# Performance work log

Measured on AMD Instinct MI355X. Metric: run time of the kernel, lower is better.

The kernel has to match this reference:

```python
import jax, jax.numpy as jnp
import numpy as np

B, T, CIN = 8, 4096, 512
GROUP, ENTRY = 2, 320
COUT = 512
D = COUT // GROUP  # per-group codebook dim = 256


def setup_inputs() -> dict:
    key = jax.random.key(0)
    k_x, k_w, k_cb, k_g = jax.random.split(key, 4)
    x = jax.random.normal(k_x, (B, T, CIN), dtype=jnp.float32)
    # weight_proj: Linear(in_channel, group*entry)
    Wp = jax.random.normal(k_w, (GROUP * ENTRY, CIN), dtype=jnp.float32) * (1.0 / np.sqrt(CIN))
    bp = jnp.zeros((GROUP * ENTRY,), dtype=jnp.float32)
    # stacked codebooks: [group, entry, out_channel//group]
    codebooks = jax.random.normal(k_cb, (GROUP, ENTRY, D), dtype=jnp.float32)
    # pre-sampled gumbel noise (torch gumbel_softmax samples this internally)
    gumbel = jax.random.gumbel(k_g, (B, T, GROUP * ENTRY), dtype=jnp.float32)
    return {"x": x, "Wp": Wp, "bp": bp, "codebooks": codebooks, "gumbel": gumbel}


def reference(x, Wp, bp, codebooks, gumbel):
    # weight_proj
    logits = jnp.einsum('btc,ec->bte', x, Wp) + bp          # [B,T,group*entry]
    # gumbel_softmax(tau=1, hard=False, dim=-1): softmax over full group*entry axis
    y = jax.nn.softmax(logits + gumbel, axis=-1)            # [B,T,group*entry]
    # chunk into groups -> contiguous reshape matches torch.chunk
    yg = y.reshape(B, T, GROUP, ENTRY)                      # [B,T,G,E]
    # per-group matmul against codebook weights, then concat over groups
    out = jnp.einsum('btge,ged->btgd', yg, codebooks)       # [B,T,G,D]
    return out.reshape(B, T, GROUP * D)                     # [B,T,out_channel]
```

## Files before the change

### kernel.cpp

```cpp
#include <hip/hip_runtime.h>
#include <hip/hip_bf16.h>
#include <stdint.h>

#define BT     32768
#define CIN    512
#define NE     640
#define ENTRY  320
#define DD     256
#define MROWS  64
#define TPB    512

using bf16x8 = __attribute__((ext_vector_type(8))) short;
using f32x4  = __attribute__((ext_vector_type(4))) float;

#define Y_OFF   0
#define Y_STR   648
#define S_OFF   82944
#define A_OFF   83200
#define A_STR   80
#define B_OFF   88320
#define CB_OFF  83200
#define SMEM_BYTES 129280

__device__ __forceinline__ unsigned short f2b(float f) {
    union { float f; uint32_t u; } v; v.f = f;
    uint32_t u = v.u;
    return (unsigned short)((u + 0x7FFFu + ((u >> 16) & 1u)) >> 16);
}

__device__ __forceinline__ void gl2lds16(const void* g, void* l) {
    __builtin_amdgcn_global_load_lds((const __attribute__((address_space(1))) void*)g,
                                     (__attribute__((address_space(3))) void*)l, 16, 0, 0);
}

__global__ void prep_kernel(const float* __restrict__ Wp, const float* __restrict__ cb,
                            unsigned short* __restrict__ WpB, unsigned short* __restrict__ cbT) {
    int i = blockIdx.x * blockDim.x + threadIdx.x;
    if (i < NE * CIN) {
        WpB[i] = f2b(Wp[i]);
    } else {
        int o = i - NE * CIN;
        if (o < 2 * ENTRY * DD) {
            int g = o / (DD * ENTRY);
            int r = o - g * (DD * ENTRY);
            int d = r / ENTRY;
            int e = r - d * ENTRY;
            cbT[o] = f2b(cb[(g * ENTRY + e) * DD + d]);
        }
    }
}

__global__ __launch_bounds__(TPB, 2) void fused_kernel(
    const float* __restrict__ x, const float* __restrict__ bp,
    const float* __restrict__ gum, const unsigned short* __restrict__ WpB,
    const unsigned short* __restrict__ cbT, float* __restrict__ out) {

    extern __shared__ char smem[];
    unsigned short* yS = (unsigned short*)(smem + Y_OFF);
    float*          sS = (float*)(smem + S_OFF);
    char*           aS = smem + A_OFF;
    char*           bS = smem + B_OFF;
    char*           cS = smem + CB_OFF;

    const int tid = threadIdx.x;
    const int w  = tid >> 6;
    const int l  = tid & 63;
    const int q  = l >> 4;
    const int ln = l & 15;
    const int rowbase = blockIdx.x * MROWS;

    if (tid < MROWS) sS[tid] = 0.0f;

    f32x4 acc1[4][5];
    const f32x4 fz = {0.f, 0.f, 0.f, 0.f};
#pragma unroll
    for (int rt = 0; rt < 4; ++rt)
#pragma unroll
        for (int ct = 0; ct < 5; ++ct) acc1[rt][ct] = fz;

    const int ar  = tid >> 3;
    const int akq = tid & 7;
    const float* xrow = x + (rowbase + ar) * CIN + akq * 4;

#pragma unroll 1
    for (int ks = 0; ks < 16; ++ks) {
        const int k0 = ks * 32;
        __syncthreads();
        float4 xv = *(const float4*)(xrow + k0);
        ushort4 hv;
        hv.x = f2b(xv.x); hv.y = f2b(xv.y); hv.z = f2b(xv.z); hv.w = f2b(xv.w);
        *(ushort4*)(aS + ar * A_STR + akq * 8) = hv;
#pragma unroll
        for (int i = 0; i < 5; ++i) {
            int cbase = i * 512 + (w << 6);
            int c = cbase + l;
            int e = c >> 2;
            int q2 = (c & 3) ^ ((e >> 1) & 3);
            gl2lds16(WpB + e * CIN + k0 + q2 * 8, bS + cbase * 16);
        }
        __syncthreads();
        bf16x8 af[4];
#pragma unroll
        for (int rt = 0; rt < 4; ++rt)
            af[rt] = *(const bf16x8*)(aS + (rt * 16 + ln) * A_STR + q * 16);
        bf16x8 bfr[5];
#pragma unroll
        for (int ct = 0; ct < 5; ++ct) {
            int e = w * 80 + ct * 16 + ln;
            int ch = e * 4 + (q ^ ((e >> 1) & 3));
            bfr[ct] = *(const bf16x8*)(bS + ch * 16);
        }
#pragma unroll
        for (int rt = 0; rt < 4; ++rt)
#pragma unroll
            for (int ct = 0; ct < 5; ++ct)
                acc1[rt][ct] = __builtin_amdgcn_mfma_f32_16x16x32_bf16(af[rt], bfr[ct], acc1[rt][ct], 0, 0, 0);
    }

    float bpv[5];
#pragma unroll
    for (int ct = 0; ct < 5; ++ct) bpv[ct] = bp[w * 80 + ct * 16 + ln];

#pragma unroll
    for (int rt = 0; rt < 4; ++rt) {
#pragma unroll
        for (int r = 0; r < 4; ++r) {
            int row = rt * 16 + q * 4 + r;
            int grow = (rowbase + row) * NE;
            float p = 0.f;
#pragma unroll
            for (int ct = 0; ct < 5; ++ct) {
                int col = w * 80 + ct * 16 + ln;
                float v = acc1[rt][ct][r] + bpv[ct] + gum[grow + col];
                float e = __expf(v);
                yS[row * Y_STR + col] = f2b(e);
                p += e;
            }
            p += __shfl_xor(p, 1);
            p += __shfl_xor(p, 2);
            p += __shfl_xor(p, 4);
            p += __shfl_xor(p, 8);
            if (ln == 0) atomicAdd(&sS[row], p);
        }
    }

    f32x4 acc2[4][4];
#pragma unroll
    for (int rt = 0; rt < 4; ++rt)
#pragma unroll
        for (int ct = 0; ct < 4; ++ct) acc2[rt][ct] = fz;

    const int g  = w >> 2;
    const int nb = (w & 3) * 64;

#pragma unroll 1
    for (int ks = 0; ks < 10; ++ks) {
        const int k0 = ks * 32;
        __syncthreads();
#pragma unroll
        for (int i = 0; i < 4; ++i) {
            int cbase = i * 512 + (w << 6);
            int c = cbase + l;
            int gg = c >> 10;
            int cc = c & 1023;
            int n = cc >> 2;
            int q2 = (cc & 3) ^ ((n >> 1) & 3);
            gl2lds16(cbT + (gg * DD + n) * ENTRY + k0 + q2 * 8, cS + cbase * 16);
        }
        __syncthreads();
        bf16x8 af[4];
#pragma unroll
        for (int rt = 0; rt < 4; ++rt)
            af[rt] = *(const bf16x8*)((char*)yS + (rt * 16 + ln) * (Y_STR * 2) + (g * ENTRY + k0 + q * 8) * 2);
        bf16x8 bfr[4];
#pragma unroll
        for (int ct = 0; ct < 4; ++ct) {
            int n = nb + ct * 16 + ln;
            int ch = (g << 10) + n * 4 + (q ^ ((n >> 1) & 3));
            bfr[ct] = *(const bf16x8*)(cS + ch * 16);
        }
#pragma unroll
        for (int rt = 0; rt < 4; ++rt)
#pragma unroll
            for (int ct = 0; ct < 4; ++ct)
                acc2[rt][ct] = __builtin_amdgcn_mfma_f32_16x16x32_bf16(af[rt], bfr[ct], acc2[rt][ct], 0, 0, 0);
    }

#pragma unroll
    for (int rt = 0; rt < 4; ++rt) {
#pragma unroll
        for (int r = 0; r < 4; ++r) {
            int row = rt * 16 + q * 4 + r;
            float inv = 1.0f / sS[row];
            int orow = (rowbase + row) * 512;
#pragma unroll
            for (int ct = 0; ct < 4; ++ct) {
                int col = g * DD + nb + ct * 16 + ln;
                out[orow + col] = acc2[rt][ct][r] * inv;
            }
        }
    }
}

extern "C" void kernel_launch(void* const* d_in, const int* in_sizes, int n_in,
                              void* d_out, int out_size, void* d_ws, size_t ws_size,
                              hipStream_t stream) {
    const float* x   = (const float*)d_in[0];
    const float* Wp  = (const float*)d_in[1];
    const float* bp  = (const float*)d_in[2];
    const float* cb  = (const float*)d_in[3];
    const float* gum = (const float*)d_in[4];
    float* out = (float*)d_out;

    unsigned short* WpB = (unsigned short*)d_ws;
    unsigned short* cbT = WpB + NE * CIN;

    int prep_total = NE * CIN + 2 * ENTRY * DD;
    prep_kernel<<<(prep_total + 255) / 256, 256, 0, stream>>>(Wp, cb, WpB, cbT);

    fused_kernel<<<dim3(BT / MROWS), dim3(TPB), SMEM_BYTES, stream>>>(x, bp, gum, WpB, cbT, out);
}
```

Measured before the change: 251.2 us.

## Stage full x tile in LDS once and stream weights directly into registers

The whole 64x512 x tile is converted to bf16 and staged into LDS once up front, replacing the per-k-step staging that needed two barriers per iteration. The Wp and codebook B-fragments are no longer copied into LDS; each wave loads them from global memory straight into registers, double-buffered one k-step ahead. Gumbel noise values are also prefetched a row ahead during the softmax epilogue. This removes most barriers and LDS traffic, at the cost of more LDS (150KB, which limits occupancy to one block per CU) and redundant global or L2 reads of the weights across waves.

```diff
diff --git a/kernel.cpp b/kernel.cpp
--- a/kernel.cpp
+++ b/kernel.cpp
@@ -12,25 +12,20 @@
 
 using bf16x8 = __attribute__((ext_vector_type(8))) short;
 using f32x4  = __attribute__((ext_vector_type(4))) float;
-
-#define Y_OFF   0
-#define Y_STR   648
-#define S_OFF   82944
-#define A_OFF   83200
-#define A_STR   80
-#define B_OFF   88320
-#define CB_OFF  83200
-#define SMEM_BYTES 129280
+using u16x8  = __attribute__((ext_vector_type(8))) unsigned short;
+
+#define X_OFF   0
+#define X_STRB  1040
+#define Y_OFF   66560
+#define Y_STRB  1296
+#define Y_STRE  648
+#define S_OFF   149504
+#define SMEM_BYTES 149760
 
 __device__ __forceinline__ unsigned short f2b(float f) {
     union { float f; uint32_t u; } v; v.f = f;
     uint32_t u = v.u;
     return (unsigned short)((u + 0x7FFFu + ((u >> 16) & 1u)) >> 16);
-}
-
-__device__ __forceinline__ void gl2lds16(const void* g, void* l) {
-    __builtin_amdgcn_global_load_lds((const __attribute__((address_space(1))) void*)g,
-                                     (__attribute__((address_space(3))) void*)l, 16, 0, 0);
 }
 
 __global__ void prep_kernel(const float* __restrict__ Wp, const float* __restrict__ cb,
@@ -58,9 +53,6 @@
     extern __shared__ char smem[];
     unsigned short* yS = (unsigned short*)(smem + Y_OFF);
     float*          sS = (float*)(smem + S_OFF);
-    char*           aS = smem + A_OFF;
-    char*           bS = smem + B_OFF;
-    char*           cS = smem + CB_OFF;
 
     const int tid = threadIdx.x;
     const int w  = tid >> 6;
@@ -71,78 +63,96 @@
 
     if (tid < MROWS) sS[tid] = 0.0f;
 
+#pragma unroll
+    for (int i = 0; i < 8; ++i) {
+        int c   = tid + i * TPB;
+        int row = c >> 6;
+        int c8  = c & 63;
+        const float* p = x + (size_t)(rowbase + row) * CIN + c8 * 8;
+        float4 a = *(const float4*)p;
+        float4 b = *(const float4*)(p + 4);
+        u16x8 hv;
+        hv[0] = f2b(a.x); hv[1] = f2b(a.y); hv[2] = f2b(a.z); hv[3] = f2b(a.w);
+        hv[4] = f2b(b.x); hv[5] = f2b(b.y); hv[6] = f2b(b.z); hv[7] = f2b(b.w);
+        *(u16x8*)(smem + X_OFF + row * X_STRB + c8 * 16) = hv;
+    }
+
+    const float* gbase = gum + (size_t)rowbase * NE + w * 80 + ln;
+    float gv[5];
+#pragma unroll
+    for (int j = 0; j < 5; ++j) gv[j] = gbase[(size_t)(q * 4) * NE + j * 16];
+
     f32x4 acc1[4][5];
     const f32x4 fz = {0.f, 0.f, 0.f, 0.f};
 #pragma unroll
     for (int rt = 0; rt < 4; ++rt)
 #pragma unroll
-        for (int ct = 0; ct < 5; ++ct) acc1[rt][ct] = fz;
-
-    const int ar  = tid >> 3;
-    const int akq = tid & 7;
-    const float* xrow = x + (rowbase + ar) * CIN + akq * 4;
+        for (int j = 0; j < 5; ++j) acc1[rt][j] = fz;
+
+    const unsigned short* bp1 = WpB + (size_t)(w * 80 + ln) * CIN + q * 8;
+    bf16x8 bc[5], bn[5];
+#pragma unroll
+    for (int j = 0; j < 5; ++j) bc[j] = *(const bf16x8*)(bp1 + (size_t)j * 16 * CIN);
+
+    __syncthreads();
 
 #pragma unroll 1
     for (int ks = 0; ks < 16; ++ks) {
         const int k0 = ks * 32;
-        __syncthreads();
-        float4 xv = *(const float4*)(xrow + k0);
-        ushort4 hv;
-        hv.x = f2b(xv.x); hv.y = f2b(xv.y); hv.z = f2b(xv.z); hv.w = f2b(xv.w);
-        *(ushort4*)(aS + ar * A_STR + akq * 8) = hv;
-#pragma unroll
-        for (int i = 0; i < 5; ++i) {
-            int cbase = i * 512 + (w << 6);
-            int c = cbase + l;
-            int e = c >> 2;
-            int q2 = (c & 3) ^ ((e >> 1) & 3);
-            gl2lds16(WpB + e * CIN + k0 + q2 * 8, bS + cbase * 16);
-        }
-        __syncthreads();
+        if (ks < 15) {
+#pragma unroll
+            for (int j = 0; j < 5; ++j)
+                bn[j] = *(const bf16x8*)(bp1 + (size_t)j * 16 * CIN + k0 + 32);
+        }
         bf16x8 af[4];
 #pragma unroll
         for (int rt = 0; rt < 4; ++rt)
-            af[rt] = *(const bf16x8*)(aS + (rt * 16 + ln) * A_STR + q * 16);
-        bf16x8 bfr[5];
-#pragma unroll
-        for (int ct = 0; ct < 5; ++ct) {
-            int e = w * 80 + ct * 16 + ln;
-            int ch = e * 4 + (q ^ ((e >> 1) & 3));
-            bfr[ct] = *(const bf16x8*)(bS + ch * 16);
-        }
-#pragma unroll
-        for (int rt = 0; rt < 4; ++rt)
-#pragma unroll
-            for (int ct = 0; ct < 5; ++ct)
-                acc1[rt][ct] = __builtin_amdgcn_mfma_f32_16x16x32_bf16(af[rt], bfr[ct], acc1[rt][ct], 0, 0, 0);
+            af[rt] = *(const bf16x8*)(smem + X_OFF + (rt * 16 + ln) * X_STRB + (k0 + q * 8) * 2);
+#pragma unroll
+        for (int j = 0; j < 5; ++j)
+#pragma unroll
+            for (int rt = 0; rt < 4; ++rt)
+                acc1[rt][j] = __builtin_amdgcn_mfma_f32_16x16x32_bf16(af[rt], bc[j], acc1[rt][j], 0, 0, 0);
+        if (ks < 15) {
+#pragma unroll
+            for (int j = 0; j < 5; ++j) bc[j] = bn[j];
+        }
     }
 
     float bpv[5];
 #pragma unroll
-    for (int ct = 0; ct < 5; ++ct) bpv[ct] = bp[w * 80 + ct * 16 + ln];
-
-#pragma unroll
-    for (int rt = 0; rt < 4; ++rt) {
-#pragma unroll
-        for (int r = 0; r < 4; ++r) {
-            int row = rt * 16 + q * 4 + r;
-            int grow = (rowbase + row) * NE;
-            float p = 0.f;
-#pragma unroll
-            for (int ct = 0; ct < 5; ++ct) {
-                int col = w * 80 + ct * 16 + ln;
-                float v = acc1[rt][ct][r] + bpv[ct] + gum[grow + col];
-                float e = __expf(v);
-                yS[row * Y_STR + col] = f2b(e);
-                p += e;
-            }
-            p += __shfl_xor(p, 1);
-            p += __shfl_xor(p, 2);
-            p += __shfl_xor(p, 4);
-            p += __shfl_xor(p, 8);
-            if (ln == 0) atomicAdd(&sS[row], p);
-        }
-    }
+    for (int j = 0; j < 5; ++j) bpv[j] = bp[w * 80 + j * 16 + ln];
+
+#pragma unroll
+    for (int ri = 0; ri < 16; ++ri) {
+        float gn[5];
+        if (ri < 15) {
+            int nrow = ((ri + 1) >> 2) * 16 + q * 4 + ((ri + 1) & 3);
+            const float* pn = gbase + (size_t)nrow * NE;
+#pragma unroll
+            for (int j = 0; j < 5; ++j) gn[j] = pn[j * 16];
+        }
+        const int rt = ri >> 2, r = ri & 3;
+        const int row = rt * 16 + q * 4 + r;
+        float p = 0.f;
+#pragma unroll
+        for (int j = 0; j < 5; ++j) {
+            float v = acc1[rt][j][r] + bpv[j] + gv[j];
+            float e = __expf(v);
+            yS[row * Y_STRE + w * 80 + j * 16 + ln] = f2b(e);
+            p += e;
+        }
+        p += __shfl_xor(p, 1);
+        p += __shfl_xor(p, 2);
+        p += __shfl_xor(p, 4);
+        p += __shfl_xor(p, 8);
+        if (ln == 0) atomicAdd(&sS[row], p);
+#pragma unroll
+        for (int j = 0; j < 5; ++j) gv[j] = gn[j];
+    }
+
+    const int g   = w >> 2;
+    const int nbp = (w & 3) * 64;
 
     f32x4 acc2[4][4];
 #pragma unroll
@@ -150,54 +160,46 @@
 #pragma unroll
         for (int ct = 0; ct < 4; ++ct) acc2[rt][ct] = fz;
 
-    const int g  = w >> 2;
-    const int nb = (w & 3) * 64;
+    const unsigned short* cp = cbT + (size_t)(g * DD + nbp + ln) * ENTRY + q * 8;
+    bf16x8 cc[4], cn[4];
+#pragma unroll
+    for (int ct = 0; ct < 4; ++ct) cc[ct] = *(const bf16x8*)(cp + (size_t)ct * 16 * ENTRY);
+
+    __syncthreads();
 
 #pragma unroll 1
     for (int ks = 0; ks < 10; ++ks) {
         const int k0 = ks * 32;
-        __syncthreads();
-#pragma unroll
-        for (int i = 0; i < 4; ++i) {
-            int cbase = i * 512 + (w << 6);
-            int c = cbase + l;
-            int gg = c >> 10;
-            int cc = c & 1023;
-            int n = cc >> 2;
-            int q2 = (cc & 3) ^ ((n >> 1) & 3);
-            gl2lds16(cbT + (gg * DD + n) * ENTRY + k0 + q2 * 8, cS + cbase * 16);
-        }
-        __syncthreads();
-        bf16x8 af[4];
+        if (ks < 9) {
+#pragma unroll
+            for (int ct = 0; ct < 4; ++ct)
+                cn[ct] = *(const bf16x8*)(cp + (size_t)ct * 16 * ENTRY + k0 + 32);
+        }
+        bf16x8 af2[4];
 #pragma unroll
         for (int rt = 0; rt < 4; ++rt)
-            af[rt] = *(const bf16x8*)((char*)yS + (rt * 16 + ln) * (Y_STR * 2) + (g * ENTRY + k0 + q * 8) * 2);
-        bf16x8 bfr[4];
-#pragma unroll
-        for (int ct = 0; ct < 4; ++ct) {
-            int n = nb + ct * 16 + ln;
-            int ch = (g << 10) + n * 4 + (q ^ ((n >> 1) & 3));
-            bfr[ct] = *(const bf16x8*)(cS + ch * 16);
-        }
-#pragma unroll
-        for (int rt = 0; rt < 4; ++rt)
+            af2[rt] = *(const bf16x8*)(smem + Y_OFF + (rt * 16 + ln) * Y_STRB + (g * ENTRY + k0 + q * 8) * 2);
+#pragma unroll
+        for (int ct = 0; ct < 4; ++ct)
+#pragma unroll
+            for (int rt = 0; rt < 4; ++rt)
+                acc2[rt][ct] = __builtin_amdgcn_mfma_f32_16x16x32_bf16(af2[rt], cc[ct], acc2[rt][ct], 0, 0, 0);
+        if (ks < 9) {
+#pragma unroll
+            for (int ct = 0; ct < 4; ++ct) cc[ct] = cn[ct];
+        }
+    }
+
+#pragma unroll
+    for (int rt = 0; rt < 4; ++rt) {
+#pragma unroll
+        for (int r = 0; r < 4; ++r) {
+            const int row = rt * 16 + q * 4 + r;
+            const float inv = 1.0f / sS[row];
+            float* op = out + (size_t)(rowbase + row) * 512 + g * DD + nbp + ln;
 #pragma unroll
             for (int ct = 0; ct < 4; ++ct)
-                acc2[rt][ct] = __builtin_amdgcn_mfma_f32_16x16x32_bf16(af[rt], bfr[ct], acc2[rt][ct], 0, 0, 0);
-    }
-
-#pragma unroll
-    for (int rt = 0; rt < 4; ++rt) {
-#pragma unroll
-        for (int r = 0; r < 4; ++r) {
-            int row = rt * 16 + q * 4 + r;
-            float inv = 1.0f / sS[row];
-            int orow = (rowbase + row) * 512;
-#pragma unroll
-            for (int ct = 0; ct < 4; ++ct) {
-                int col = g * DD + nb + ct * 16 + ln;
-                out[orow + col] = acc2[rt][ct][r] * inv;
-            }
+                op[ct * 16] = acc2[rt][ct][r] * inv;
         }
     }
 }
```

Result: no change. 251.1 us (-0.0%).
